# Optimization experiments

Measured on AMD Instinct MI355X. Metric: run time of the kernel, lower is better.

The kernel has to match this reference:

```python
import jax, jax.numpy as jnp
import numpy as np

N = 100000   # nodes
E = 1600000  # edges
D_IN, D_H, D_OUT = 128, 128, 40


def setup_inputs() -> dict:
    key = jax.random.key(0)
    ks = jax.random.split(key, 12)
    feat = jax.random.normal(ks[0], (N, D_IN), dtype=jnp.float32)
    edge_src = jax.random.randint(ks[1], (E,), 0, N, dtype=jnp.int32)
    edge_dst = jax.random.randint(ks[2], (E,), 0, N, dtype=jnp.int32)
    s = 0.05
    W0 = jax.random.normal(ks[3], (D_IN, D_H), dtype=jnp.float32) * s
    W1 = jax.random.normal(ks[4], (D_H, D_H), dtype=jnp.float32) * s
    W2 = jax.random.normal(ks[5], (D_H, D_OUT), dtype=jnp.float32) * s
    b2 = jnp.zeros((D_OUT,), dtype=jnp.float32)
    g0 = jnp.ones((D_H,), dtype=jnp.float32)
    beta0 = jnp.zeros((D_H,), dtype=jnp.float32)
    g1 = jnp.ones((D_H,), dtype=jnp.float32)
    beta1 = jnp.zeros((D_H,), dtype=jnp.float32)
    return dict(feat=feat, edge_src=edge_src, edge_dst=edge_dst,
                W0=W0, W1=W1, W2=W2, b2=b2,
                g0=g0, beta0=beta0, g1=g1, beta1=beta1)


def _degree_norms(edge_src, edge_dst):
    ones = jnp.ones((E,), dtype=jnp.float32)
    out_deg = jax.ops.segment_sum(ones, edge_src, num_segments=N)
    in_deg = jax.ops.segment_sum(ones, edge_dst, num_segments=N)
    # DGL GraphConv norm='both': clamp degree to >=1, pow(-0.5)
    ns = jnp.where(out_deg < 1.0, 1.0, out_deg) ** -0.5  # src norm
    nd = jnp.where(in_deg < 1.0, 1.0, in_deg) ** -0.5    # dst norm
    return ns, nd


def _gcn_conv(h, W, edge_src, edge_dst, ns, nd, bias=None):
    # norm='both': scale src, project (W first since out<=in), aggregate, scale dst
    h = (h * ns[:, None]) @ W                       # [N, out]
    msg = jnp.take(h, edge_src, axis=0)             # [E, out] gather
    agg = jax.ops.segment_sum(msg, edge_dst, num_segments=N)  # scatter-add
    agg = agg * nd[:, None]
    if bias is not None:
        agg = agg + bias
    return agg


def _bn(x, gamma, beta, eps=1e-5):
    mean = jnp.mean(x, axis=0)
    var = jnp.var(x, axis=0)
    return (x - mean) * jax.lax.rsqrt(var + eps) * gamma + beta


def reference(feat, edge_src, edge_dst, W0, W1, W2, b2, g0, beta0, g1, beta1):
    ns, nd = _degree_norms(edge_src, edge_dst)
    # dropout layers are identity in eval mode
    h = _gcn_conv(feat, W0, edge_src, edge_dst, ns, nd)
    h = jax.nn.relu(_bn(h, g0, beta0))
    h = _gcn_conv(h, W1, edge_src, edge_dst, ns, nd)
    h = jax.nn.relu(_bn(h, g1, beta1))
    h = _gcn_conv(h, W2, edge_src, edge_dst, ns, nd, bias=b2)
    return h
```

## Files before the change

### kernel.cpp

```cpp
#include <hip/hip_runtime.h>
#include <hip/hip_bf16.h>


#define D_H 128
#define SCAN_CHUNK 1024

typedef unsigned int uint32;
typedef unsigned short ushort16;
typedef __attribute__((ext_vector_type(8))) short short8v;
typedef __attribute__((ext_vector_type(4))) float float4v;

__device__ __forceinline__ ushort16 f2bf(float f) {
    union { float f; uint32 u; } v;
    v.f = f;
    uint32 u = v.u;
    return (ushort16)((u + 0x7fffu + ((u >> 16) & 1u)) >> 16);
}
__device__ __forceinline__ float2 bf2f2(uint32 u) {
    union { uint32 i; float f; } a, b;
    a.i = u << 16;
    b.i = u & 0xffff0000u;
    return make_float2(a.f, b.f);
}

__global__ __launch_bounds__(256) void bucket_count2_kernel(
    const int* __restrict__ src, const int* __restrict__ dst,
    int* __restrict__ M, int* __restrict__ M2, int E, int nbuck) {
    __shared__ int h[512], h2[512];
    for (int i = threadIdx.x; i < nbuck; i += 256) { h[i] = 0; h2[i] = 0; }
    __syncthreads();
    int j = blockIdx.x;
    int epb = (E + 127) >> 7;
    int estart = j * epb, eend = min(estart + epb, E);
    for (int e = estart + threadIdx.x; e < eend; e += 256) {
        atomicAdd(&h[dst[e] >> 8], 1);
        atomicAdd(&h2[src[e] >> 8], 1);
    }
    __syncthreads();
    for (int b = threadIdx.x; b < nbuck; b += 256) {
        M[(size_t)b * 128 + j] = h[b];
        M2[(size_t)b * 128 + j] = h2[b];
    }
}

__global__ __launch_bounds__(256) void scan1f_kernel(
    const int* __restrict__ M, const int* __restrict__ M2,
    int* __restrict__ bsum, int g, int n) {
    int half = (blockIdx.x >= g) ? 1 : 0;
    int blk = blockIdx.x - half * g;
    const int* deg = half ? M2 : M;
    int tid = threadIdx.x;
    int base = blk * SCAN_CHUNK + tid * 4;
    int4 v = make_int4(0, 0, 0, 0);
    if (base + 3 < n) {
        v = *(const int4*)(deg + base);
    } else {
        if (base + 0 < n) v.x = deg[base + 0];
        if (base + 1 < n) v.y = deg[base + 1];
        if (base + 2 < n) v.z = deg[base + 2];
        if (base + 3 < n) v.w = deg[base + 3];
    }
    int s = v.x + v.y + v.z + v.w;
    __shared__ int red[256];
    red[tid] = s;
    __syncthreads();
#pragma unroll
    for (int off = 128; off > 0; off >>= 1) {
        if (tid < off) red[tid] += red[tid + off];
        __syncthreads();
    }
    if (tid == 0) bsum[blockIdx.x] = red[0];
}

__global__ __launch_bounds__(256) void scan3f_kernel(
    const int* __restrict__ M, const int* __restrict__ M2,
    const int* __restrict__ bsum, int* __restrict__ Mx, int* __restrict__ Mx2,
    int g, int n) {
    int half = (blockIdx.x >= g) ? 1 : 0;
    int blk = blockIdx.x - half * g;
    const int* deg = half ? M2 : M;
    int* outp = half ? Mx2 : Mx;
    int tid = threadIdx.x;
    int base = blk * SCAN_CHUNK + tid * 4;
    int4 v = make_int4(0, 0, 0, 0);
    if (base + 3 < n) {
        v = *(const int4*)(deg + base);
    } else {
        if (base + 0 < n) v.x = deg[base + 0];
        if (base + 1 < n) v.y = deg[base + 1];
        if (base + 2 < n) v.z = deg[base + 2];
        if (base + 3 < n) v.w = deg[base + 3];
    }
    int s = v.x + v.y + v.z + v.w;

    __shared__ int bs[128];
    if (tid < 128) bs[tid] = (tid < g) ? bsum[half * g + tid] : 0;
    __syncthreads();
#pragma unroll
    for (int off = 1; off < 128; off <<= 1) {
        int t = (tid < 128 && tid >= off) ? bs[tid - off] : 0;
        __syncthreads();
        if (tid < 128) bs[tid] += t;
        __syncthreads();
    }
    int blockbase = (blk == 0) ? 0 : bs[blk - 1];
    int total = bs[g - 1];

    __shared__ int sc[256];
    sc[tid] = s;
    __syncthreads();
#pragma unroll
    for (int off = 1; off < 256; off <<= 1) {
        int t = (tid >= off) ? sc[tid - off] : 0;
        __syncthreads();
        sc[tid] += t;
        __syncthreads();
    }
    int excl = sc[tid] - s + blockbase;
    int p0 = excl;
    int p1 = p0 + v.x;
    int p2 = p1 + v.y;
    int p3 = p2 + v.z;
    if (base + 3 < n) {
        *(int4*)(outp + base) = make_int4(p0, p1, p2, p3);
    } else {
        if (base + 0 < n) outp[base + 0] = p0;
        if (base + 1 < n) outp[base + 1] = p1;
        if (base + 2 < n) outp[base + 2] = p2;
    }
    if (blk == g - 1 && tid == 0) outp[n] = total;
}

__global__ __launch_bounds__(256) void bucket_scatter2_kernel(
    const int* __restrict__ src, const int* __restrict__ dst,
    const int* __restrict__ Mx, const int* __restrict__ Mx2,
    uint32* __restrict__ packed, uint32* __restrict__ sp, int E, int nbuck) {
    __shared__ int cb1[512], c1[512], cb2[512], c2[512];
    int j = blockIdx.x;
    for (int i = threadIdx.x; i < nbuck; i += 256) {
        cb1[i] = Mx[(size_t)i * 128 + j];
        c1[i] = 0;
        cb2[i] = Mx2[(size_t)i * 128 + j];
        c2[i] = 0;
    }
    __syncthreads();
    int epb = (E + 127) >> 7;
    int estart = j * epb, eend = min(estart + epb, E);
    for (int e = estart + threadIdx.x; e < eend; e += 256) {
        int s = src[e], d = dst[e];
        int b = d >> 8;
        int r = atomicAdd(&c1[b], 1);
        packed[cb1[b] + r] = ((uint32)s << 8) | (uint32)(d & 255);
        int b2 = s >> 8;
        int r2 = atomicAdd(&c2[b2], 1);
        sp[cb2[b2] + r2] = (uint32)s;
    }
}

__global__ __launch_bounds__(256) void csr_src_kernel(
    const uint32* __restrict__ packed, const int* __restrict__ Mx,
    const uint32* __restrict__ sp, const int* __restrict__ Mx2,
    int* __restrict__ row_ptr, float* __restrict__ nd, float* __restrict__ ns,
    int* __restrict__ ssrc, int E, int N, int nbuck) {
    __shared__ int cnt[256], pos0[256], cur[256], sc[256], cnt2[256];
    int b = blockIdx.x, tid = threadIdx.x;
    int lo = Mx[(size_t)b * 128];
    int hi = (b == nbuck - 1) ? E : Mx[(size_t)(b + 1) * 128];
    int lo2 = Mx2[(size_t)b * 128];
    int hi2 = (b == nbuck - 1) ? E : Mx2[(size_t)(b + 1) * 128];
    cnt[tid] = 0;
    cur[tid] = 0;
    cnt2[tid] = 0;
    __syncthreads();
    for (int e = lo + tid; e < hi; e += 256)
        atomicAdd(&cnt[packed[e] & 255u], 1);
    for (int e = lo2 + tid; e < hi2; e += 256)
        atomicAdd(&cnt2[sp[e] & 255u], 1);
    __syncthreads();
    int c = cnt[tid];
    sc[tid] = c;
    __syncthreads();
#pragma unroll
    for (int off = 1; off < 256; off <<= 1) {
        int t = (tid >= off) ? sc[tid - off] : 0;
        __syncthreads();
        sc[tid] += t;
        __syncthreads();
    }
    int excl = sc[tid] - c;
    pos0[tid] = lo + excl;
    int node = b * 256 + tid;
    if (node < N) {
        row_ptr[node] = lo + excl;
        nd[node] = rsqrtf((float)max(c, 1));
        ns[node] = rsqrtf((float)max(cnt2[tid], 1));
    }
    if (b == 0 && tid == 0) row_ptr[N] = E;
    __syncthreads();
    for (int e = lo + tid; e < hi; e += 256) {
        uint32 p = packed[e];
        int local = (int)(p & 255u);
        int r = atomicAdd(&cur[local], 1);
        ssrc[pos0[local] + r] = (int)(p >> 8);
    }
}

__global__ void prepw_kernel(const float* __restrict__ W0, const float* __restrict__ W1,
                             const float* __restrict__ W2,
                             ushort16* __restrict__ Wt0, ushort16* __restrict__ Wt1,
                             ushort16* __restrict__ Wt2) {
    int idx = blockIdx.x * 256 + threadIdx.x;
    if (idx < 16384) {
        int n = idx & 127, k = idx >> 7;
        Wt0[n * 128 + k] = f2bf(W0[k * 128 + n]);
        Wt1[n * 128 + k] = f2bf(W1[k * 128 + n]);
    } else {
        int i2 = idx - 16384;
        int n = i2 >> 7, k = i2 & 127;
        Wt2[n * 128 + k] = (n < 40) ? f2bf(W2[k * 40 + n]) : (ushort16)0;
    }
}

template <bool XBF16, bool FUSE_BN>
__global__ __launch_bounds__(256) void gemm_mfma_kernel(
    const void* __restrict__ Xv, const ushort16* __restrict__ Wt,
    const float* __restrict__ ns, const float* __restrict__ stats,
    const float* __restrict__ gamma, const float* __restrict__ beta,
    float invn, ushort16* __restrict__ Yb, int nrows) {
    constexpr int LDK = 72;
    __shared__ short As[128 * LDK];
    __shared__ short Ws[128 * LDK];
    __shared__ float abl[256];
    int tid = threadIdx.x;
    int row0 = blockIdx.x * 128;
    int wave = tid >> 6, lane = tid & 63;
    int wm = (wave >> 1) * 64, wn = (wave & 1) * 64;
    int l15 = lane & 15, quad = lane >> 4;
    float4v acc[4][4] = {{}};

    if (FUSE_BN) {
        if (tid < 128) {
            float mean = stats[tid] * invn;
            float var = stats[128 + tid] * invn - mean * mean;
            float a = rsqrtf(var + 1e-5f) * gamma[tid];
            abl[tid] = a;
            abl[128 + tid] = beta[tid] - mean * a;
        }
        __syncthreads();
    }

#pragma unroll
    for (int p = 0; p < 2; ++p) {
        int k0 = p * 64;
        {
            int srow = tid >> 1;
            int half = (tid & 1) * 32;
            int grow = row0 + srow;
            bool ok = grow < nrows;
            float sc = ok ? ns[grow] : 0.f;
            uint32 outu[16];
            if (XBF16) {
                const uint4* xp = (const uint4*)((const uint32*)Xv +
                                                 (size_t)grow * 64 + ((k0 + half) >> 1));
                uint4 u4[4];
#pragma unroll
                for (int q = 0; q < 4; ++q)
                    u4[q] = ok ? xp[q] : make_uint4(0, 0, 0, 0);
                const uint32* uu = (const uint32*)u4;
#pragma unroll
                for (int j = 0; j < 16; ++j) {
                    float2 f = bf2f2(uu[j]);
                    if (FUSE_BN) {
                        int c = k0 + half + j * 2;
                        f.x = fmaxf(fmaf(f.x, abl[c], abl[128 + c]), 0.f);
                        f.y = fmaxf(fmaf(f.y, abl[c + 1], abl[128 + c + 1]), 0.f);
                    }
                    outu[j] = (uint32)f2bf(f.x * sc) | ((uint32)f2bf(f.y * sc) << 16);
                }
            } else {
                const float4* xp = (const float4*)((const float*)Xv +
                                                   (size_t)grow * 128 + k0 + half);
                float4 f4[8];
#pragma unroll
                for (int q = 0; q < 8; ++q)
                    f4[q] = ok ? xp[q] : make_float4(0.f, 0.f, 0.f, 0.f);
                const float* ff = (const float*)f4;
#pragma unroll
                for (int j = 0; j < 16; ++j) {
                    float fx = ff[2 * j], fy = ff[2 * j + 1];
                    outu[j] = (uint32)f2bf(fx * sc) | ((uint32)f2bf(fy * sc) << 16);
                }
            }
            uint4* dstA = (uint4*)&As[srow * LDK + half];
#pragma unroll
            for (int q = 0; q < 4; ++q) dstA[q] = ((uint4*)outu)[q];
            const uint4* wp = (const uint4*)((const uint32*)Wt +
                                             srow * 64 + ((k0 + half) >> 1));
            uint4* dstW = (uint4*)&Ws[srow * LDK + half];
#pragma unroll
            for (int q = 0; q < 4; ++q) dstW[q] = wp[q];
        }
        __syncthreads();
#pragma unroll
        for (int ks = 0; ks < 2; ++ks) {
            int koff = ks * 32 + quad * 8;
            short8v a[4], b[4];
#pragma unroll
            for (int t = 0; t < 4; ++t)
                a[t] = *(const short8v*)&As[(wm + t * 16 + l15) * LDK + koff];
#pragma unroll
            for (int u = 0; u < 4; ++u)
                b[u] = *(const short8v*)&Ws[(wn + u * 16 + l15) * LDK + koff];
#pragma unroll
            for (int t = 0; t < 4; ++t)
#pragma unroll
                for (int u = 0; u < 4; ++u)
                    acc[t][u] = __builtin_amdgcn_mfma_f32_16x16x32_bf16(
                        a[t], b[u], acc[t][u], 0, 0, 0);
        }
        __syncthreads();
    }
#pragma unroll
    for (int t = 0; t < 4; ++t) {
#pragma unroll
        for (int r = 0; r < 4; ++r) {
            int grow = row0 + wm + t * 16 + quad * 4 + r;
            if (grow < nrows) {
#pragma unroll
                for (int u = 0; u < 4; ++u)
                    Yb[(size_t)grow * 128 + wn + u * 16 + l15] = f2bf(acc[t][u][r]);
            }
        }
    }
}

__global__ __launch_bounds__(256) void gemm_final_mfma_kernel(
    const uint32* __restrict__ Xb, const ushort16* __restrict__ Wt2,
    const float* __restrict__ bias, float* __restrict__ Y, int nrows) {
    constexpr int LDK = 72;
    __shared__ short As[128 * LDK];
    __shared__ short Ws[64 * LDK];
    int tid = threadIdx.x;
    int row0 = blockIdx.x * 128;
    int wave = tid >> 6, lane = tid & 63;
    int wm = (wave >> 1) * 64, wn = (wave & 1) * 32;
    int l15 = lane & 15, quad = lane >> 4;
    float4v acc[4][2] = {{}};

#pragma unroll
    for (int p = 0; p < 2; ++p) {
        int k0 = p * 64;
        {
            int srow = tid >> 1;
            int half = (tid & 1) * 32;
            int grow = row0 + srow;
            bool ok = grow < nrows;
            const uint4* xp = (const uint4*)(Xb + (size_t)grow * 64 + ((k0 + half) >> 1));
            uint4 u4[4];
#pragma unroll
            for (int q = 0; q < 4; ++q)
                u4[q] = ok ? xp[q] : make_uint4(0, 0, 0, 0);
            uint4* dstA = (uint4*)&As[srow * LDK + half];
#pragma unroll
            for (int q = 0; q < 4; ++q) dstA[q] = u4[q];
        }
        {
            int srow = tid >> 2;
            int off = (tid & 3) * 16;
            const uint4* wp = (const uint4*)((const uint32*)Wt2 +
                                             srow * 64 + ((k0 + off) >> 1));
            uint4* dw = (uint4*)&Ws[srow * LDK + off];
            dw[0] = wp[0];
            dw[1] = wp[1];
        }
        __syncthreads();
#pragma unroll
        for (int ks = 0; ks < 2; ++ks) {
            int koff = ks * 32 + quad * 8;
            short8v a[4], b[2];
#pragma unroll
            for (int t = 0; t < 4; ++t)
                a[t] = *(const short8v*)&As[(wm + t * 16 + l15) * LDK + koff];
#pragma unroll
            for (int u = 0; u < 2; ++u)
                b[u] = *(const short8v*)&Ws[(wn + u * 16 + l15) * LDK + koff];
#pragma unroll
            for (int t = 0; t < 4; ++t)
#pragma unroll
                for (int u = 0; u < 2; ++u)
                    acc[t][u] = __builtin_amdgcn_mfma_f32_16x16x32_bf16(
                        a[t], b[u], acc[t][u], 0, 0, 0);
        }
        __syncthreads();
    }
#pragma unroll
    for (int t = 0; t < 4; ++t) {
#pragma unroll
        for (int r = 0; r < 4; ++r) {
            int grow = row0 + wm + t * 16 + quad * 4 + r;
            if (grow < nrows) {
#pragma unroll
                for (int u = 0; u < 2; ++u) {
                    int col = wn + u * 16 + l15;
                    if (col < 40)
                        Y[(size_t)grow * 40 + col] = acc[t][u][r] + bias[col];
                }
            }
        }
    }
}

__global__ __launch_bounds__(256) void agg128_kernel(
    const uint32* __restrict__ xwb, const int* __restrict__ row_ptr,
    const int* __restrict__ ssrc, const float* __restrict__ nd,
    uint32* __restrict__ outb, int n) {
    int node = blockIdx.x * 4 + (threadIdx.x >> 6);
    if (node >= n) return;
    int lane = threadIdx.x & 63;
    int beg = row_ptr[node], end = row_ptr[node + 1];
    float x = 0.f, y = 0.f;
    int e = beg;
    for (; e + 8 <= end; e += 8) {
        int s[8];
#pragma unroll
        for (int j = 0; j < 8; ++j) s[j] = ssrc[e + j];
        uint32 u[8];
#pragma unroll
        for (int j = 0; j < 8; ++j) u[j] = xwb[(size_t)s[j] * 64 + lane];
#pragma unroll
        for (int j = 0; j < 8; ++j) {
            float2 v = bf2f2(u[j]);
            x += v.x;
            y += v.y;
        }
    }
    for (; e + 2 <= end; e += 2) {
        uint32 u0 = xwb[(size_t)ssrc[e] * 64 + lane];
        uint32 u1 = xwb[(size_t)ssrc[e + 1] * 64 + lane];
        float2 v0 = bf2f2(u0), v1 = bf2f2(u1);
        x += v0.x + v1.x;
        y += v0.y + v1.y;
    }
    if (e < end) {
        float2 v0 = bf2f2(xwb[(size_t)ssrc[e] * 64 + lane]);
        x += v0.x;
        y += v0.y;
    }
    float s = nd[node];
    outb[(size_t)node * 64 + lane] =
        (uint32)f2bf(x * s) | ((uint32)f2bf(y * s) << 16);
}

__global__ __launch_bounds__(256) void agg128_bn_kernel(
    const uint32* __restrict__ xwb, const int* __restrict__ row_ptr,
    const int* __restrict__ ssrc, const float* __restrict__ nd,
    const float* __restrict__ ns, const float* __restrict__ stats,
    const float* __restrict__ gamma, const float* __restrict__ beta,
    float invn, uint32* __restrict__ outb, int n) {
    int node = blockIdx.x * 4 + (threadIdx.x >> 6);
    if (node >= n) return;
    int lane = threadIdx.x & 63;
    int c = lane * 2;
    float m0 = stats[c] * invn, m1 = stats[c + 1] * invn;
    float v0_ = stats[128 + c] * invn - m0 * m0;
    float v1_ = stats[128 + c + 1] * invn - m1 * m1;
    float a0 = rsqrtf(v0_ + 1e-5f) * gamma[c];
    float a1 = rsqrtf(v1_ + 1e-5f) * gamma[c + 1];
    float2 a2 = make_float2(a0, a1);
    float2 b2 = make_float2(beta[c] - m0 * a0, beta[c + 1] - m1 * a1);
    int beg = row_ptr[node], end = row_ptr[node + 1];
    float x = 0.f, y = 0.f;
    int e = beg;
    for (; e + 8 <= end; e += 8) {
        int s[8];
#pragma unroll
        for (int j = 0; j < 8; ++j) s[j] = ssrc[e + j];
        uint32 u[8];
        float sc[8];
#pragma unroll
        for (int j = 0; j < 8; ++j) {
            u[j] = xwb[(size_t)s[j] * 64 + lane];
            sc[j] = ns[s[j]];
        }
#pragma unroll
        for (int j = 0; j < 8; ++j) {
            float2 v = bf2f2(u[j]);
            x += fmaxf(fmaf(v.x, a2.x, b2.x), 0.f) * sc[j];
            y += fmaxf(fmaf(v.y, a2.y, b2.y), 0.f) * sc[j];
        }
    }
    for (; e < end; ++e) {
        int s0 = ssrc[e];
        float2 v0 = bf2f2(xwb[(size_t)s0 * 64 + lane]);
        float sc0 = ns[s0];
        x += fmaxf(fmaf(v0.x, a2.x, b2.x), 0.f) * sc0;
        y += fmaxf(fmaf(v0.y, a2.y, b2.y), 0.f) * sc0;
    }
    float s = nd[node];
    outb[(size_t)node * 64 + lane] =
        (uint32)f2bf(x * s) | ((uint32)f2bf(y * s) << 16);
}

__global__ __launch_bounds__(256) void bn_reduce_kernel(const uint4* __restrict__ x4,
                                                        float* __restrict__ stats, int n) {
    int tid = threadIdx.x;
    int ctile = tid & 15;
    int rgrp = tid >> 4;
    float s[8] = {}, s2[8] = {};
    for (int r = blockIdx.x * 16 + rgrp; r < n; r += gridDim.x * 16) {
        uint4 u = x4[(size_t)r * 16 + ctile];
        uint32 uu[4] = {u.x, u.y, u.z, u.w};
#pragma unroll
        for (int q = 0; q < 4; ++q) {
            float2 v = bf2f2(uu[q]);
            s[q * 2] += v.x;
            s[q * 2 + 1] += v.y;
            s2[q * 2] = fmaf(v.x, v.x, s2[q * 2]);
            s2[q * 2 + 1] = fmaf(v.y, v.y, s2[q * 2 + 1]);
        }
    }
    __shared__ float ls[128], ls2[128];
    if (tid < 128) { ls[tid] = 0.f; ls2[tid] = 0.f; }
    __syncthreads();
#pragma unroll
    for (int j = 0; j < 8; ++j) {
        atomicAdd(&ls[ctile * 8 + j], s[j]);
        atomicAdd(&ls2[ctile * 8 + j], s2[j]);
    }
    __syncthreads();
    if (tid < 128) {
        atomicAdd(&stats[tid], ls[tid]);
        atomicAdd(&stats[128 + tid], ls2[tid]);
    }
}


extern "C" void kernel_launch(void* const* d_in, const int* in_sizes, int n_in,
                              void* d_out, int out_size, void* d_ws, size_t ws_size,
                              hipStream_t stream) {
    const float* feat = (const float*)d_in[0];
    const int* edge_src = (const int*)d_in[1];
    const int* edge_dst = (const int*)d_in[2];
    const float* W0 = (const float*)d_in[3];
    const float* W1 = (const float*)d_in[4];
    const float* W2 = (const float*)d_in[5];
    const float* b2 = (const float*)d_in[6];
    const float* g0 = (const float*)d_in[7];
    const float* beta0 = (const float*)d_in[8];
    const float* g1 = (const float*)d_in[9];
    const float* beta1 = (const float*)d_in[10];
    float* out = (float*)d_out;

    const int N = in_sizes[0] / D_H;
    const int E = in_sizes[1];
    const int nbuck = (N + 255) >> 8;
    const float invN = 1.0f / (float)N;

    char* p = (char*)d_ws;
    auto alloc = [&](size_t bytes) {
        char* r = p;
        p += (bytes + 255) & ~(size_t)255;
        return r;
    };
    uint32* Ab = (uint32*)alloc((size_t)N * D_H * 2);
    uint32* Bb = (uint32*)alloc((size_t)N * D_H * 2);
    float* ns = (float*)alloc((size_t)N * 4);
    float* nd = (float*)alloc((size_t)N * 4);
    int* row_ptr = (int*)alloc((size_t)(N + 1) * 4);
    int* ssrc = (int*)alloc((size_t)E * 4);
    uint32* packed = (uint32*)alloc((size_t)E * 4);
    uint32* sp = (uint32*)alloc((size_t)E * 4);
    int* M = (int*)alloc((size_t)nbuck * 128 * 4);
    int* Mx = (int*)alloc(((size_t)nbuck * 128 + 4) * 4);
    int* M2 = (int*)alloc((size_t)nbuck * 128 * 4);
    int* Mx2 = (int*)alloc(((size_t)nbuck * 128 + 4) * 4);
    int* bsum = (int*)alloc(256 * 4);
    float* stats0 = (float*)alloc(256 * 4);
    float* stats1 = (float*)alloc(256 * 4);
    ushort16* Wt0 = (ushort16*)alloc(128 * 128 * 2);
    ushort16* Wt1 = (ushort16*)alloc(128 * 128 * 2);
    ushort16* Wt2 = (ushort16*)alloc(64 * 128 * 2);
    (void)ws_size;

    hipMemsetAsync(stats0, 0, 2048, stream);

    const int ggrid = (N + 127) / 128;
    const int agrid = (N + 3) / 4;
    const int nM = nbuck * 128;
    const int sgridM = (nM + SCAN_CHUNK - 1) / SCAN_CHUNK;

    prepw_kernel<<<96, 256, 0, stream>>>(W0, W1, W2, Wt0, Wt1, Wt2);

    bucket_count2_kernel<<<128, 256, 0, stream>>>(edge_src, edge_dst, M, M2, E, nbuck);
    scan1f_kernel<<<2 * sgridM, 256, 0, stream>>>(M, M2, bsum, sgridM, nM);
    scan3f_kernel<<<2 * sgridM, 256, 0, stream>>>(M, M2, bsum, Mx, Mx2, sgridM, nM);
    bucket_scatter2_kernel<<<128, 256, 0, stream>>>(edge_src, edge_dst, Mx, Mx2,
                                                    packed, sp, E, nbuck);
    csr_src_kernel<<<nbuck, 256, 0, stream>>>(packed, Mx, sp, Mx2, row_ptr, nd, ns,
                                              ssrc, E, N, nbuck);

    gemm_mfma_kernel<false, false><<<ggrid, 256, 0, stream>>>(
        feat, Wt0, ns, nullptr, nullptr, nullptr, invN, (ushort16*)Bb, N);
    agg128_kernel<<<agrid, 256, 0, stream>>>(Bb, row_ptr, ssrc, nd, Ab, N);
    bn_reduce_kernel<<<512, 256, 0, stream>>>((const uint4*)Ab, stats0, N);

    gemm_mfma_kernel<true, true><<<ggrid, 256, 0, stream>>>(
        Ab, Wt1, ns, stats0, g0, beta0, invN, (ushort16*)Bb, N);
    agg128_kernel<<<agrid, 256, 0, stream>>>(Bb, row_ptr, ssrc, nd, Ab, N);
    bn_reduce_kernel<<<512, 256, 0, stream>>>((const uint4*)Ab, stats1, N);

    agg128_bn_kernel<<<agrid, 256, 0, stream>>>(Ab, row_ptr, ssrc, nd, ns,
                                                stats1, g1, beta1, invN, Bb, N);
    gemm_final_mfma_kernel<<<ggrid, 256, 0, stream>>>(Bb, Wt2, b2, out, N);
}
```

Before: 495.7 us.

## Reorder final layer to project before aggregating, gathering 64-wide rows

The last GCN layer now applies BN+ReLU+src-norm inside the GEMM's A-tile load and projects to 40 (padded 64) bf16 columns first, then aggregates the narrow projected rows with a half-wave-per-edge gather kernel that adds dst-norm and bias. This replaces gathering 128-wide rows over 1.6M edges with gathering 64-wide rows, halving gather traffic in the last aggregation. It adds per-element BN math in the GEMM load path and an extra bf16 rounding of the projected values before summation.

New measurement: 468.6 us. 5.5% less time.

```diff
diff --git a/kernel.cpp b/kernel.cpp
--- a/kernel.cpp
+++ b/kernel.cpp
@@ -334,18 +334,30 @@
     }
 }
 
-__global__ __launch_bounds__(256) void gemm_final_mfma_kernel(
+__global__ __launch_bounds__(256) void gemm_mfma2_kernel(
     const uint32* __restrict__ Xb, const ushort16* __restrict__ Wt2,
-    const float* __restrict__ bias, float* __restrict__ Y, int nrows) {
+    const float* __restrict__ ns, const float* __restrict__ stats,
+    const float* __restrict__ gamma, const float* __restrict__ beta,
+    float invn, ushort16* __restrict__ Y2b, int nrows) {
     constexpr int LDK = 72;
     __shared__ short As[128 * LDK];
     __shared__ short Ws[64 * LDK];
+    __shared__ float abl[256];
     int tid = threadIdx.x;
     int row0 = blockIdx.x * 128;
     int wave = tid >> 6, lane = tid & 63;
     int wm = (wave >> 1) * 64, wn = (wave & 1) * 32;
     int l15 = lane & 15, quad = lane >> 4;
     float4v acc[4][2] = {{}};
+
+    if (tid < 128) {
+        float mean = stats[tid] * invn;
+        float var = stats[128 + tid] * invn - mean * mean;
+        float a = rsqrtf(var + 1e-5f) * gamma[tid];
+        abl[tid] = a;
+        abl[128 + tid] = beta[tid] - mean * a;
+    }
+    __syncthreads();
 
 #pragma unroll
     for (int p = 0; p < 2; ++p) {
@@ -355,14 +367,25 @@
             int half = (tid & 1) * 32;
             int grow = row0 + srow;
             bool ok = grow < nrows;
+            float sc = ok ? ns[grow] : 0.f;
             const uint4* xp = (const uint4*)(Xb + (size_t)grow * 64 + ((k0 + half) >> 1));
             uint4 u4[4];
 #pragma unroll
             for (int q = 0; q < 4; ++q)
                 u4[q] = ok ? xp[q] : make_uint4(0, 0, 0, 0);
+            const uint32* uu = (const uint32*)u4;
+            uint32 outu[16];
+#pragma unroll
+            for (int j = 0; j < 16; ++j) {
+                float2 f = bf2f2(uu[j]);
+                int c = k0 + half + j * 2;
+                f.x = fmaxf(fmaf(f.x, abl[c], abl[128 + c]), 0.f);
+                f.y = fmaxf(fmaf(f.y, abl[c + 1], abl[128 + c + 1]), 0.f);
+                outu[j] = (uint32)f2bf(f.x * sc) | ((uint32)f2bf(f.y * sc) << 16);
+            }
             uint4* dstA = (uint4*)&As[srow * LDK + half];
 #pragma unroll
-            for (int q = 0; q < 4; ++q) dstA[q] = u4[q];
+            for (int q = 0; q < 4; ++q) dstA[q] = ((uint4*)outu)[q];
         }
         {
             int srow = tid >> 2;
@@ -400,11 +423,8 @@
             int grow = row0 + wm + t * 16 + quad * 4 + r;
             if (grow < nrows) {
 #pragma unroll
-                for (int u = 0; u < 2; ++u) {
-                    int col = wn + u * 16 + l15;
-                    if (col < 40)
-                        Y[(size_t)grow * 40 + col] = acc[t][u][r] + bias[col];
-                }
+                for (int u = 0; u < 2; ++u)
+                    Y2b[(size_t)grow * 64 + wn + u * 16 + l15] = f2bf(acc[t][u][r]);
             }
         }
     }
@@ -451,54 +471,52 @@
         (uint32)f2bf(x * s) | ((uint32)f2bf(y * s) << 16);
 }
 
-__global__ __launch_bounds__(256) void agg128_bn_kernel(
-    const uint32* __restrict__ xwb, const int* __restrict__ row_ptr,
+__global__ __launch_bounds__(256) void agg40_kernel(
+    const uint32* __restrict__ y2b, const int* __restrict__ row_ptr,
     const int* __restrict__ ssrc, const float* __restrict__ nd,
-    const float* __restrict__ ns, const float* __restrict__ stats,
-    const float* __restrict__ gamma, const float* __restrict__ beta,
-    float invn, uint32* __restrict__ outb, int n) {
+    const float* __restrict__ bias, float* __restrict__ out, int n) {
     int node = blockIdx.x * 4 + (threadIdx.x >> 6);
     if (node >= n) return;
     int lane = threadIdx.x & 63;
-    int c = lane * 2;
-    float m0 = stats[c] * invn, m1 = stats[c + 1] * invn;
-    float v0_ = stats[128 + c] * invn - m0 * m0;
-    float v1_ = stats[128 + c + 1] * invn - m1 * m1;
-    float a0 = rsqrtf(v0_ + 1e-5f) * gamma[c];
-    float a1 = rsqrtf(v1_ + 1e-5f) * gamma[c + 1];
-    float2 a2 = make_float2(a0, a1);
-    float2 b2 = make_float2(beta[c] - m0 * a0, beta[c + 1] - m1 * a1);
+    int l32 = lane & 31;
+    int par = lane >> 5;
     int beg = row_ptr[node], end = row_ptr[node + 1];
     float x = 0.f, y = 0.f;
     int e = beg;
     for (; e + 8 <= end; e += 8) {
-        int s[8];
-#pragma unroll
-        for (int j = 0; j < 8; ++j) s[j] = ssrc[e + j];
-        uint32 u[8];
-        float sc[8];
-#pragma unroll
-        for (int j = 0; j < 8; ++j) {
-            u[j] = xwb[(size_t)s[j] * 64 + lane];
-            sc[j] = ns[s[j]];
-        }
-#pragma unroll
-        for (int j = 0; j < 8; ++j) {
+        int s[4];
+#pragma unroll
+        for (int j = 0; j < 4; ++j) s[j] = ssrc[e + 2 * j + par];
+        uint32 u[4];
+#pragma unroll
+        for (int j = 0; j < 4; ++j) u[j] = y2b[(size_t)s[j] * 32 + l32];
+#pragma unroll
+        for (int j = 0; j < 4; ++j) {
             float2 v = bf2f2(u[j]);
-            x += fmaxf(fmaf(v.x, a2.x, b2.x), 0.f) * sc[j];
-            y += fmaxf(fmaf(v.y, a2.y, b2.y), 0.f) * sc[j];
-        }
-    }
-    for (; e < end; ++e) {
-        int s0 = ssrc[e];
-        float2 v0 = bf2f2(xwb[(size_t)s0 * 64 + lane]);
-        float sc0 = ns[s0];
-        x += fmaxf(fmaf(v0.x, a2.x, b2.x), 0.f) * sc0;
-        y += fmaxf(fmaf(v0.y, a2.y, b2.y), 0.f) * sc0;
-    }
-    float s = nd[node];
-    outb[(size_t)node * 64 + lane] =
-        (uint32)f2bf(x * s) | ((uint32)f2bf(y * s) << 16);
+            x += v.x;
+            y += v.y;
+        }
+    }
+    for (; e + 2 <= end; e += 2) {
+        uint32 u0 = y2b[(size_t)ssrc[e + par] * 32 + l32];
+        float2 v = bf2f2(u0);
+        x += v.x;
+        y += v.y;
+    }
+    if (e < end && par == 0) {
+        float2 v = bf2f2(y2b[(size_t)ssrc[e] * 32 + l32]);
+        x += v.x;
+        y += v.y;
+    }
+    x += __shfl_down(x, 32, 64);
+    y += __shfl_down(y, 32, 64);
+    if (par == 0 && l32 < 20) {
+        float s = nd[node];
+        int c = l32 * 2;
+        float2 bb = *(const float2*)&bias[c];
+        *(float2*)(out + (size_t)node * 40 + c) =
+            make_float2(fmaf(x, s, bb.x), fmaf(y, s, bb.y));
+    }
 }
 
 __global__ __launch_bounds__(256) void bn_reduce_kernel(const uint4* __restrict__ x4,
@@ -609,7 +627,7 @@
     agg128_kernel<<<agrid, 256, 0, stream>>>(Bb, row_ptr, ssrc, nd, Ab, N);
     bn_reduce_kernel<<<512, 256, 0, stream>>>((const uint4*)Ab, stats1, N);
 
-    agg128_bn_kernel<<<agrid, 256, 0, stream>>>(Ab, row_ptr, ssrc, nd, ns,
-                                                stats1, g1, beta1, invN, Bb, N);
-    gemm_final_mfma_kernel<<<ggrid, 256, 0, stream>>>(Bb, Wt2, b2, out, N);
-}
+    gemm_mfma2_kernel<<<ggrid, 256, 0, stream>>>(
+        Ab, Wt2, ns, stats1, g1, beta1, invN, (ushort16*)Bb, N);
+    agg40_kernel<<<agrid, 256, 0, stream>>>(Bb, row_ptr, ssrc, nd, b2, out, N);
+}
```
